# Performance work log

Measured on AMD Instinct MI355X. Metric: run time of the kernel, lower is better.

Reference implementation:

```python
import jax, jax.numpy as jnp
import numpy as np

STRIDE = 32
WINDOW = 16


def setup_inputs() -> dict:
    key = jax.random.key(0)
    kq, kk, kv = jax.random.split(key, 3)
    B, H, S, D = 1, 16, 2048, 64
    q = jax.random.normal(kq, (B, H, S, D), dtype=jnp.float32)
    k = jax.random.normal(kk, (B, H, S, D), dtype=jnp.float32)
    v = jax.random.normal(kv, (B, H, S, D), dtype=jnp.float32)
    return {"q": q, "k": k, "v": v}


def _strided_attention(q, k, v, stride=STRIDE, w=WINDOW):
    b, h, n, d = q.shape
    scale = jnp.asarray(1.0 / np.sqrt(d), dtype=q.dtype)

    # strided (global) tokens: indices 0, stride, 2*stride, ...  [S_str]
    str_idx = jnp.arange(0, n, stride)
    k_str = k[:, :, str_idx, :]  # [b,h,S_str,d]
    v_str = v[:, :, str_idx, :]

    # local window gather: token i attends to j in [i-w, i+w]  (L = 2w+1 slots)
    offs = jnp.arange(-w, w + 1)                      # [L]
    pos = jnp.arange(n)[:, None] + offs[None, :]      # [n, L]
    local_valid = (pos >= 0) & (pos < n)              # [n, L]
    pos_c = jnp.clip(pos, 0, n - 1)
    k_loc = k[:, :, pos_c, :]                         # [b,h,n,L,d]
    v_loc = v[:, :, pos_c, :]                         # [b,h,n,L,d]

    # In the original, strided keys are concatenated ONLY when start > 0,
    # i.e. when i > w (since strided_indices[0] == 0 is inside the window
    # whenever start == 0). Duplicates (strided token inside the local
    # window) are intentionally kept, matching torch.cat semantics.
    use_str = jnp.arange(n) > w                       # [n]

    sc_loc = jnp.einsum('bhnd,bhnld->bhnl', q, k_loc) * scale
    sc_loc = jnp.where(local_valid[None, None], sc_loc, -jnp.inf)
    sc_str = jnp.einsum('bhnd,bhsd->bhns', q, k_str) * scale
    sc_str = jnp.where(use_str[None, None, :, None], sc_str, -jnp.inf)

    L = offs.shape[0]
    attn = jax.nn.softmax(jnp.concatenate([sc_loc, sc_str], axis=-1), axis=-1)
    attn = jnp.nan_to_num(attn, nan=0.0)
    a_loc, a_str = attn[..., :L], attn[..., L:]

    out = jnp.einsum('bhnl,bhnld->bhnd', a_loc, v_loc) \
        + jnp.einsum('bhns,bhsd->bhnd', a_str, v_str)
    return out


def reference(q, k, v):
    return _strided_attention(q, k, v)
```

## Files before the change

### kernel.cpp

```cpp
#include <hip/hip_runtime.h>
#include <math.h>


typedef __attribute__((ext_vector_type(8))) short bf16x8;
typedef __attribute__((ext_vector_type(4))) float f32x4;

constexpr int H = 16, S = 2048, D = 64, W = 16;
constexpr int QB    = 64;
constexpr int NLOC  = 96;
constexpr int NROWS = 160;
constexpr int NT    = 10;
constexpr float SCALE = 0.125f;

constexpr int QSTR = 72;
constexpr int VSTR = 168;
constexpr int QHI  = 0;
constexpr int QLO  = QHI + QB * QSTR;
constexpr int KB   = QLO + QB * QSTR;
constexpr int VTB  = 0;
constexpr int LDS_U = KB + NROWS * QSTR;

__device__ __forceinline__ ushort f2bf(float x) {
    union { float f; unsigned u; } t; t.f = x;
    unsigned r = t.u + 0x7fffu + ((t.u >> 16) & 1u);
    return (ushort)(r >> 16);
}
__device__ __forceinline__ float bf2f(ushort b) {
    union { float f; unsigned u; } t; t.u = ((unsigned)b) << 16;
    return t.f;
}
__device__ __forceinline__ unsigned pk2(float a, float b) {
    return (unsigned)f2bf(a) | ((unsigned)f2bf(b) << 16);
}
__device__ __forceinline__ int rowpos(int r, int n0) {
    if (r < NLOC) {
        int p = n0 - W + r;
        return p < 0 ? 0 : (p > S - 1 ? S - 1 : p);
    }
    return (r - NLOC) * 32;
}

__global__ __launch_bounds__(256, 2) void strided_attn_mfma(
    const float* __restrict__ q,
    const float* __restrict__ k,
    const float* __restrict__ v,
    float* __restrict__ out)
{
    __shared__ ushort lds[LDS_U];

    const int tid  = threadIdx.x;
    const int w    = tid >> 6;
    const int lane = tid & 63;
    const int c    = lane & 15;
    const int g    = lane >> 4;
    const int bid  = blockIdx.x;
    const int swz  = (bid & 7) * 64 + (bid >> 3);
    const int h    = swz >> 5;
    const int n0   = (swz & 31) << 6;

    const float* __restrict__ qh = q + (size_t)(h * S) * D;
    const float* __restrict__ kh = k + (size_t)(h * S) * D;
    const float* __restrict__ vh = v + (size_t)(h * S) * D;

    const int ntask = (tid < 128) ? 3 : 2;
    float4 vreg[3][4];
#pragma unroll
    for (int tt = 0; tt < 3; ++tt) {
        if (tt < ntask) {
            const int tau = tid + (tt << 8);
            const int rp = tau % 80, ch = tau / 80;
            const float* s0 = vh + (size_t)rowpos(2 * rp,     n0) * D + ch * 8;
            const float* s1 = vh + (size_t)rowpos(2 * rp + 1, n0) * D + ch * 8;
            vreg[tt][0] = *(const float4*)s0;
            vreg[tt][1] = *(const float4*)(s0 + 4);
            vreg[tt][2] = *(const float4*)s1;
            vreg[tt][3] = *(const float4*)(s1 + 4);
        }
    }

    for (int t = tid; t < 1792; t += 256) {
        if (t < 512) {
            const int row = t >> 3, ch = t & 7;
            const float* src = qh + (size_t)(n0 + row) * D + ch * 8;
            const float4 a = *(const float4*)src;
            const float4 b = *(const float4*)(src + 4);
            const float xs[8] = {a.x, a.y, a.z, a.w, b.x, b.y, b.z, b.w};
            union { bf16x8 v; ushort u[8]; } hi, lo;
#pragma unroll
            for (int j = 0; j < 8; ++j) {
                const ushort hb = f2bf(xs[j]);
                hi.u[j] = hb;
                lo.u[j] = f2bf(xs[j] - bf2f(hb));
            }
            *(bf16x8*)&lds[QHI + row * QSTR + ch * 8] = hi.v;
            *(bf16x8*)&lds[QLO + row * QSTR + ch * 8] = lo.v;
        } else {
            const int u = t - 512;
            const int row = u >> 3, ch = u & 7;
            const float* src = kh + (size_t)rowpos(row, n0) * D + ch * 8;
            const float4 a = *(const float4*)src;
            const float4 b = *(const float4*)(src + 4);
            const float xs[8] = {a.x, a.y, a.z, a.w, b.x, b.y, b.z, b.w};
            union { bf16x8 v; ushort u[8]; } hi;
#pragma unroll
            for (int j = 0; j < 8; ++j) hi.u[j] = f2bf(xs[j]);
            *(bf16x8*)&lds[KB + row * QSTR + ch * 8] = hi.v;
        }
    }

    unsigned vpk[3][8];
#pragma unroll
    for (int tt = 0; tt < 3; ++tt) {
        if (tt < ntask) {
            const float r0[8] = {vreg[tt][0].x, vreg[tt][0].y, vreg[tt][0].z, vreg[tt][0].w,
                                 vreg[tt][1].x, vreg[tt][1].y, vreg[tt][1].z, vreg[tt][1].w};
            const float r1[8] = {vreg[tt][2].x, vreg[tt][2].y, vreg[tt][2].z, vreg[tt][2].w,
                                 vreg[tt][3].x, vreg[tt][3].y, vreg[tt][3].z, vreg[tt][3].w};
#pragma unroll
            for (int j = 0; j < 8; ++j) vpk[tt][j] = pk2(r0[j], r1[j]);
        }
    }
    __syncthreads();

    const int qb = w * 16;
    const int qi = qb + c;
    const int nq = n0 + qi;
    const int qa = (qb + c) * QSTR + g * 8;
    const bf16x8 bQH0 = *(bf16x8*)&lds[QHI + qa];
    const bf16x8 bQH1 = *(bf16x8*)&lds[QHI + qa + 32];
    const bf16x8 bQL0 = *(bf16x8*)&lds[QLO + qa];
    const bf16x8 bQL1 = *(bf16x8*)&lds[QLO + qa + 32];

    f32x4 acc[NT];
#pragma unroll
    for (int t = 0; t < NT; ++t) acc[t] = (f32x4){0.f, 0.f, 0.f, 0.f};
#pragma unroll
    for (int t = 0; t < NT; ++t) {
        const int kb = KB + (t * 16 + c) * QSTR + g * 8;
        const bf16x8 a0 = *(bf16x8*)&lds[kb];
        const bf16x8 a1 = *(bf16x8*)&lds[kb + 32];
        f32x4 a4 = acc[t];
        a4 = __builtin_amdgcn_mfma_f32_16x16x32_bf16(a0, bQH0, a4, 0, 0, 0);
        a4 = __builtin_amdgcn_mfma_f32_16x16x32_bf16(a1, bQH1, a4, 0, 0, 0);
        a4 = __builtin_amdgcn_mfma_f32_16x16x32_bf16(a0, bQL0, a4, 0, 0, 0);
        a4 = __builtin_amdgcn_mfma_f32_16x16x32_bf16(a1, bQL1, a4, 0, 0, 0);
        acc[t] = a4;
    }

    float p[NT][4];
#pragma unroll
    for (int t = 0; t < 6; ++t) {
#pragma unroll
        for (int i = 0; i < 4; ++i) {
            const int j = t * 16 + 4 * g + i;
            const bool ok = ((unsigned)(j - qi) <= 32u) &&
                            ((unsigned)(n0 - W + j) < (unsigned)S);
            p[t][i] = ok ? acc[t][i] * SCALE : -INFINITY;
        }
    }
    const bool us = nq > W;
#pragma unroll
    for (int t = 6; t < NT; ++t)
#pragma unroll
        for (int i = 0; i < 4; ++i)
            p[t][i] = us ? acc[t][i] * SCALE : -INFINITY;

    float m = -INFINITY;
#pragma unroll
    for (int t = 0; t < NT; ++t)
#pragma unroll
        for (int i = 0; i < 4; ++i) m = fmaxf(m, p[t][i]);
    m = fmaxf(m, __shfl_xor(m, 16));
    m = fmaxf(m, __shfl_xor(m, 32));

    float l = 0.f;
#pragma unroll
    for (int t = 0; t < NT; ++t)
#pragma unroll
        for (int i = 0; i < 4; ++i) { p[t][i] = __expf(p[t][i] - m); l += p[t][i]; }
    l += __shfl_xor(l, 16);
    l += __shfl_xor(l, 32);
    const float inv = 1.0f / l;

    union { bf16x8 v; unsigned u[4]; } pa[5];
#pragma unroll
    for (int kt = 0; kt < 5; ++kt) {
        pa[kt].u[0] = pk2(p[2 * kt][0] * inv,     p[2 * kt][1] * inv);
        pa[kt].u[1] = pk2(p[2 * kt][2] * inv,     p[2 * kt][3] * inv);
        pa[kt].u[2] = pk2(p[2 * kt + 1][0] * inv, p[2 * kt + 1][1] * inv);
        pa[kt].u[3] = pk2(p[2 * kt + 1][2] * inv, p[2 * kt + 1][3] * inv);
    }

    __syncthreads();

#pragma unroll
    for (int tt = 0; tt < 3; ++tt) {
        if (tt < ntask) {
            const int tau = tid + (tt << 8);
            const int rp = tau % 80, ch = tau / 80;
            const int kk = 2 * rp;
            const int kt = kk >> 5, rem = kk & 31;
            const int slot = kt * 32 + ((rem >> 2) & 3) * 8 + (rem >> 4) * 4 + (rem & 3);
#pragma unroll
            for (int j = 0; j < 8; ++j)
                *(unsigned*)&lds[VTB + (ch * 8 + j) * VSTR + slot] = vpk[tt][j];
        }
    }
    __syncthreads();

    f32x4 o[4];
#pragma unroll
    for (int dt = 0; dt < 4; ++dt) o[dt] = (f32x4){0.f, 0.f, 0.f, 0.f};
#pragma unroll
    for (int kt = 0; kt < 5; ++kt) {
#pragma unroll
        for (int dt = 0; dt < 4; ++dt) {
            const bf16x8 vb = *(bf16x8*)&lds[VTB + (dt * 16 + c) * VSTR + kt * 32 + g * 8];
            o[dt] = __builtin_amdgcn_mfma_f32_16x16x32_bf16(pa[kt].v, vb, o[dt], 0, 0, 0);
        }
    }

#pragma unroll
    for (int i = 0; i < 4; ++i) {
        const int n = n0 + qb + 4 * g + i;
        float* op = out + ((size_t)(h * S) + n) * D + c;
#pragma unroll
        for (int dt = 0; dt < 4; ++dt) op[dt * 16] = o[dt][i];
    }
}

extern "C" void kernel_launch(void* const* d_in, const int* in_sizes, int n_in,
                              void* d_out, int out_size, void* d_ws, size_t ws_size,
                              hipStream_t stream) {
    (void)in_sizes; (void)n_in; (void)d_ws; (void)ws_size; (void)out_size;
    const float* q = (const float*)d_in[0];
    const float* k = (const float*)d_in[1];
    const float* v = (const float*)d_in[2];
    float* out     = (float*)d_out;

    dim3 grid(H * (S / QB));
    dim3 block(256);
    strided_attn_mfma<<<grid, block, 0, stream>>>(q, k, v, out);
}
```

Before: 15.33 us.

## Load Q and K fragments directly from global into MFMA registers, skip LDS staging

```diff
diff --git a/kernel.cpp b/kernel.cpp
--- a/kernel.cpp
+++ b/kernel.cpp
@@ -6,19 +6,13 @@
 typedef __attribute__((ext_vector_type(4))) float f32x4;
 
 constexpr int H = 16, S = 2048, D = 64, W = 16;
-constexpr int QB    = 64;
-constexpr int NLOC  = 96;
-constexpr int NROWS = 160;
-constexpr int NT    = 10;
-constexpr float SCALE = 0.125f;
-
-constexpr int QSTR = 72;
-constexpr int VSTR = 168;
-constexpr int QHI  = 0;
-constexpr int QLO  = QHI + QB * QSTR;
-constexpr int KB   = QLO + QB * QSTR;
-constexpr int VTB  = 0;
-constexpr int LDS_U = KB + NROWS * QSTR;
+constexpr int QB   = 64;
+constexpr int NLOC = 96;
+constexpr int NT   = 10;
+constexpr float S2 = 0.18033688011112042f;
+
+constexpr int VSTR  = 168;
+constexpr int LDS_U = D * VSTR;
 
 __device__ __forceinline__ ushort f2bf(float x) {
     union { float f; unsigned u; } t; t.f = x;
@@ -31,6 +25,24 @@
 }
 __device__ __forceinline__ unsigned pk2(float a, float b) {
     return (unsigned)f2bf(a) | ((unsigned)f2bf(b) << 16);
+}
+__device__ __forceinline__ bf16x8 cvt8(const float4& a, const float4& b) {
+    union { bf16x8 v; unsigned u[4]; } r;
+    r.u[0] = pk2(a.x, a.y); r.u[1] = pk2(a.z, a.w);
+    r.u[2] = pk2(b.x, b.y); r.u[3] = pk2(b.z, b.w);
+    return r.v;
+}
+__device__ __forceinline__ void cvt_hilo(const float4& a, const float4& b,
+                                         bf16x8& hi, bf16x8& lo) {
+    const float xs[8] = {a.x, a.y, a.z, a.w, b.x, b.y, b.z, b.w};
+    union { bf16x8 v; ushort u[8]; } Hv, Lv;
+#pragma unroll
+    for (int j = 0; j < 8; ++j) {
+        const ushort hb = f2bf(xs[j]);
+        Hv.u[j] = hb;
+        Lv.u[j] = f2bf(xs[j] - bf2f(hb));
+    }
+    hi = Hv.v; lo = Lv.v;
 }
 __device__ __forceinline__ int rowpos(int r, int n0) {
     if (r < NLOC) {
@@ -78,34 +90,44 @@
         }
     }
 
-    for (int t = tid; t < 1792; t += 256) {
-        if (t < 512) {
-            const int row = t >> 3, ch = t & 7;
-            const float* src = qh + (size_t)(n0 + row) * D + ch * 8;
-            const float4 a = *(const float4*)src;
-            const float4 b = *(const float4*)(src + 4);
-            const float xs[8] = {a.x, a.y, a.z, a.w, b.x, b.y, b.z, b.w};
-            union { bf16x8 v; ushort u[8]; } hi, lo;
-#pragma unroll
-            for (int j = 0; j < 8; ++j) {
-                const ushort hb = f2bf(xs[j]);
-                hi.u[j] = hb;
-                lo.u[j] = f2bf(xs[j] - bf2f(hb));
-            }
-            *(bf16x8*)&lds[QHI + row * QSTR + ch * 8] = hi.v;
-            *(bf16x8*)&lds[QLO + row * QSTR + ch * 8] = lo.v;
+    const int qb = w * 16;
+    const int qi = qb + c;
+    const int nq = n0 + qi;
+    const float* qrow = qh + (size_t)(n0 + qb + c) * D;
+    const float4 qv00 = *(const float4*)(qrow + g * 8);
+    const float4 qv01 = *(const float4*)(qrow + g * 8 + 4);
+    const float4 qv10 = *(const float4*)(qrow + 32 + g * 8);
+    const float4 qv11 = *(const float4*)(qrow + 32 + g * 8 + 4);
+    bf16x8 bQH0, bQL0, bQH1, bQL1;
+    cvt_hilo(qv00, qv01, bQH0, bQL0);
+    cvt_hilo(qv10, qv11, bQH1, bQL1);
+
+    f32x4 acc[NT];
+#pragma unroll
+    for (int t = 0; t < NT; ++t) acc[t] = (f32x4){0.f, 0.f, 0.f, 0.f};
+
+#pragma unroll
+    for (int t = 0; t < NT; ++t) {
+        int pos;
+        if (t < 6) {
+            const int p = n0 - W + 16 * t + c;
+            pos = p < 0 ? 0 : (p > S - 1 ? S - 1 : p);
         } else {
-            const int u = t - 512;
-            const int row = u >> 3, ch = u & 7;
-            const float* src = kh + (size_t)rowpos(row, n0) * D + ch * 8;
-            const float4 a = *(const float4*)src;
-            const float4 b = *(const float4*)(src + 4);
-            const float xs[8] = {a.x, a.y, a.z, a.w, b.x, b.y, b.z, b.w};
-            union { bf16x8 v; ushort u[8]; } hi;
-#pragma unroll
-            for (int j = 0; j < 8; ++j) hi.u[j] = f2bf(xs[j]);
-            *(bf16x8*)&lds[KB + row * QSTR + ch * 8] = hi.v;
-        }
+            pos = (16 * (t - 6) + c) * 32;
+        }
+        const float* kr = kh + (size_t)pos * D;
+        const float4 k00 = *(const float4*)(kr + g * 8);
+        const float4 k01 = *(const float4*)(kr + g * 8 + 4);
+        const float4 k10 = *(const float4*)(kr + 32 + g * 8);
+        const float4 k11 = *(const float4*)(kr + 32 + g * 8 + 4);
+        const bf16x8 a0 = cvt8(k00, k01);
+        const bf16x8 a1 = cvt8(k10, k11);
+        f32x4 a4 = acc[t];
+        a4 = __builtin_amdgcn_mfma_f32_16x16x32_bf16(a0, bQH0, a4, 0, 0, 0);
+        a4 = __builtin_amdgcn_mfma_f32_16x16x32_bf16(a1, bQH1, a4, 0, 0, 0);
+        a4 = __builtin_amdgcn_mfma_f32_16x16x32_bf16(a0, bQL0, a4, 0, 0, 0);
+        a4 = __builtin_amdgcn_mfma_f32_16x16x32_bf16(a1, bQL1, a4, 0, 0, 0);
+        acc[t] = a4;
     }
 
     unsigned vpk[3][8];
@@ -120,79 +142,6 @@
             for (int j = 0; j < 8; ++j) vpk[tt][j] = pk2(r0[j], r1[j]);
         }
     }
-    __syncthreads();
-
-    const int qb = w * 16;
-    const int qi = qb + c;
-    const int nq = n0 + qi;
-    const int qa = (qb + c) * QSTR + g * 8;
-    const bf16x8 bQH0 = *(bf16x8*)&lds[QHI + qa];
-    const bf16x8 bQH1 = *(bf16x8*)&lds[QHI + qa + 32];
-    const bf16x8 bQL0 = *(bf16x8*)&lds[QLO + qa];
-    const bf16x8 bQL1 = *(bf16x8*)&lds[QLO + qa + 32];
-
-    f32x4 acc[NT];
-#pragma unroll
-    for (int t = 0; t < NT; ++t) acc[t] = (f32x4){0.f, 0.f, 0.f, 0.f};
-#pragma unroll
-    for (int t = 0; t < NT; ++t) {
-        const int kb = KB + (t * 16 + c) * QSTR + g * 8;
-        const bf16x8 a0 = *(bf16x8*)&lds[kb];
-        const bf16x8 a1 = *(bf16x8*)&lds[kb + 32];
-        f32x4 a4 = acc[t];
-        a4 = __builtin_amdgcn_mfma_f32_16x16x32_bf16(a0, bQH0, a4, 0, 0, 0);
-        a4 = __builtin_amdgcn_mfma_f32_16x16x32_bf16(a1, bQH1, a4, 0, 0, 0);
-        a4 = __builtin_amdgcn_mfma_f32_16x16x32_bf16(a0, bQL0, a4, 0, 0, 0);
-        a4 = __builtin_amdgcn_mfma_f32_16x16x32_bf16(a1, bQL1, a4, 0, 0, 0);
-        acc[t] = a4;
-    }
-
-    float p[NT][4];
-#pragma unroll
-    for (int t = 0; t < 6; ++t) {
-#pragma unroll
-        for (int i = 0; i < 4; ++i) {
-            const int j = t * 16 + 4 * g + i;
-            const bool ok = ((unsigned)(j - qi) <= 32u) &&
-                            ((unsigned)(n0 - W + j) < (unsigned)S);
-            p[t][i] = ok ? acc[t][i] * SCALE : -INFINITY;
-        }
-    }
-    const bool us = nq > W;
-#pragma unroll
-    for (int t = 6; t < NT; ++t)
-#pragma unroll
-        for (int i = 0; i < 4; ++i)
-            p[t][i] = us ? acc[t][i] * SCALE : -INFINITY;
-
-    float m = -INFINITY;
-#pragma unroll
-    for (int t = 0; t < NT; ++t)
-#pragma unroll
-        for (int i = 0; i < 4; ++i) m = fmaxf(m, p[t][i]);
-    m = fmaxf(m, __shfl_xor(m, 16));
-    m = fmaxf(m, __shfl_xor(m, 32));
-
-    float l = 0.f;
-#pragma unroll
-    for (int t = 0; t < NT; ++t)
-#pragma unroll
-        for (int i = 0; i < 4; ++i) { p[t][i] = __expf(p[t][i] - m); l += p[t][i]; }
-    l += __shfl_xor(l, 16);
-    l += __shfl_xor(l, 32);
-    const float inv = 1.0f / l;
-
-    union { bf16x8 v; unsigned u[4]; } pa[5];
-#pragma unroll
-    for (int kt = 0; kt < 5; ++kt) {
-        pa[kt].u[0] = pk2(p[2 * kt][0] * inv,     p[2 * kt][1] * inv);
-        pa[kt].u[1] = pk2(p[2 * kt][2] * inv,     p[2 * kt][3] * inv);
-        pa[kt].u[2] = pk2(p[2 * kt + 1][0] * inv, p[2 * kt + 1][1] * inv);
-        pa[kt].u[3] = pk2(p[2 * kt + 1][2] * inv, p[2 * kt + 1][3] * inv);
-    }
-
-    __syncthreads();
-
 #pragma unroll
     for (int tt = 0; tt < 3; ++tt) {
         if (tt < ntask) {
@@ -203,9 +152,54 @@
             const int slot = kt * 32 + ((rem >> 2) & 3) * 8 + (rem >> 4) * 4 + (rem & 3);
 #pragma unroll
             for (int j = 0; j < 8; ++j)
-                *(unsigned*)&lds[VTB + (ch * 8 + j) * VSTR + slot] = vpk[tt][j];
-        }
-    }
+                *(unsigned*)&lds[(ch * 8 + j) * VSTR + slot] = vpk[tt][j];
+        }
+    }
+
+    float p[NT][4];
+#pragma unroll
+    for (int t = 0; t < 6; ++t) {
+#pragma unroll
+        for (int i = 0; i < 4; ++i) {
+            const int j = t * 16 + 4 * g + i;
+            const bool ok = ((unsigned)(j - qi) <= 32u) &&
+                            ((unsigned)(n0 - W + j) < (unsigned)S);
+            p[t][i] = ok ? acc[t][i] * S2 : -INFINITY;
+        }
+    }
+    const bool us = nq > W;
+#pragma unroll
+    for (int t = 6; t < NT; ++t)
+#pragma unroll
+        for (int i = 0; i < 4; ++i)
+            p[t][i] = us ? acc[t][i] * S2 : -INFINITY;
+
+    float m = -INFINITY;
+#pragma unroll
+    for (int t = 0; t < NT; ++t)
+#pragma unroll
+        for (int i = 0; i < 4; ++i) m = fmaxf(m, p[t][i]);
+    m = fmaxf(m, __shfl_xor(m, 16));
+    m = fmaxf(m, __shfl_xor(m, 32));
+
+    float l = 0.f;
+#pragma unroll
+    for (int t = 0; t < NT; ++t)
+#pragma unroll
+        for (int i = 0; i < 4; ++i) { p[t][i] = exp2f(p[t][i] - m); l += p[t][i]; }
+    l += __shfl_xor(l, 16);
+    l += __shfl_xor(l, 32);
+    const float inv = 1.0f / l;
+
+    union { bf16x8 v; unsigned u[4]; } pa[5];
+#pragma unroll
+    for (int kt = 0; kt < 5; ++kt) {
+        pa[kt].u[0] = pk2(p[2 * kt][0] * inv,     p[2 * kt][1] * inv);
+        pa[kt].u[1] = pk2(p[2 * kt][2] * inv,     p[2 * kt][3] * inv);
+        pa[kt].u[2] = pk2(p[2 * kt + 1][0] * inv, p[2 * kt + 1][1] * inv);
+        pa[kt].u[3] = pk2(p[2 * kt + 1][2] * inv, p[2 * kt + 1][3] * inv);
+    }
+
     __syncthreads();
 
     f32x4 o[4];
@@ -215,7 +209,7 @@
     for (int kt = 0; kt < 5; ++kt) {
 #pragma unroll
         for (int dt = 0; dt < 4; ++dt) {
-            const bf16x8 vb = *(bf16x8*)&lds[VTB + (dt * 16 + c) * VSTR + kt * 32 + g * 8];
+            const bf16x8 vb = *(bf16x8*)&lds[(dt * 16 + c) * VSTR + kt * 32 + g * 8];
             o[dt] = __builtin_amdgcn_mfma_f32_16x16x32_bf16(pa[kt].v, vb, o[dt], 0, 0, 0);
         }
     }
```

Measured after the change: 23.28 us. +51.9%, slower.

## Halve query tile to 32 rows, fold scale into Q, use exp2

Applied to the files above, without the earlier changes.

```diff
diff --git a/kernel.cpp b/kernel.cpp
--- a/kernel.cpp
+++ b/kernel.cpp
@@ -6,14 +6,14 @@
 typedef __attribute__((ext_vector_type(4))) float f32x4;
 
 constexpr int H = 16, S = 2048, D = 64, W = 16;
-constexpr int QB    = 64;
-constexpr int NLOC  = 96;
-constexpr int NROWS = 160;
-constexpr int NT    = 10;
-constexpr float SCALE = 0.125f;
+constexpr int QB    = 32;
+constexpr int NLOC  = 64;
+constexpr int NROWS = 128;
+constexpr int NT    = 8;
+constexpr float S2 = 0.18033688011112042f;
 
 constexpr int QSTR = 72;
-constexpr int VSTR = 168;
+constexpr int VSTR = 136;
 constexpr int QHI  = 0;
 constexpr int QLO  = QHI + QB * QSTR;
 constexpr int KB   = QLO + QB * QSTR;
@@ -32,6 +32,12 @@
 __device__ __forceinline__ unsigned pk2(float a, float b) {
     return (unsigned)f2bf(a) | ((unsigned)f2bf(b) << 16);
 }
+__device__ __forceinline__ bf16x8 cvt8(const float4& a, const float4& b) {
+    union { bf16x8 v; unsigned u[4]; } r;
+    r.u[0] = pk2(a.x, a.y); r.u[1] = pk2(a.z, a.w);
+    r.u[2] = pk2(b.x, b.y); r.u[3] = pk2(b.z, b.w);
+    return r.v;
+}
 __device__ __forceinline__ int rowpos(int r, int n0) {
     if (r < NLOC) {
         int p = n0 - W + r;
@@ -40,7 +46,7 @@
     return (r - NLOC) * 32;
 }
 
-__global__ __launch_bounds__(256, 2) void strided_attn_mfma(
+__global__ __launch_bounds__(128, 2) void strided_attn_mfma(
     const float* __restrict__ q,
     const float* __restrict__ k,
     const float* __restrict__ v,
@@ -54,37 +60,35 @@
     const int c    = lane & 15;
     const int g    = lane >> 4;
     const int bid  = blockIdx.x;
-    const int swz  = (bid & 7) * 64 + (bid >> 3);
-    const int h    = swz >> 5;
-    const int n0   = (swz & 31) << 6;
+    const int swz  = (bid & 7) * 128 + (bid >> 3);
+    const int h    = swz >> 6;
+    const int n0   = (swz & 63) << 5;
 
     const float* __restrict__ qh = q + (size_t)(h * S) * D;
     const float* __restrict__ kh = k + (size_t)(h * S) * D;
     const float* __restrict__ vh = v + (size_t)(h * S) * D;
 
-    const int ntask = (tid < 128) ? 3 : 2;
-    float4 vreg[3][4];
-#pragma unroll
-    for (int tt = 0; tt < 3; ++tt) {
-        if (tt < ntask) {
-            const int tau = tid + (tt << 8);
-            const int rp = tau % 80, ch = tau / 80;
-            const float* s0 = vh + (size_t)rowpos(2 * rp,     n0) * D + ch * 8;
-            const float* s1 = vh + (size_t)rowpos(2 * rp + 1, n0) * D + ch * 8;
-            vreg[tt][0] = *(const float4*)s0;
-            vreg[tt][1] = *(const float4*)(s0 + 4);
-            vreg[tt][2] = *(const float4*)s1;
-            vreg[tt][3] = *(const float4*)(s1 + 4);
-        }
-    }
-
-    for (int t = tid; t < 1792; t += 256) {
-        if (t < 512) {
+    float4 vreg[4][4];
+#pragma unroll
+    for (int tt = 0; tt < 4; ++tt) {
+        const int tau = tid + (tt << 7);
+        const int rp = tau & 63, ch = tau >> 6;
+        const float* s0 = vh + (size_t)rowpos(2 * rp,     n0) * D + ch * 8;
+        const float* s1 = vh + (size_t)rowpos(2 * rp + 1, n0) * D + ch * 8;
+        vreg[tt][0] = *(const float4*)s0;
+        vreg[tt][1] = *(const float4*)(s0 + 4);
+        vreg[tt][2] = *(const float4*)s1;
+        vreg[tt][3] = *(const float4*)(s1 + 4);
+    }
+
+    for (int t = tid; t < 1280; t += 128) {
+        if (t < 256) {
             const int row = t >> 3, ch = t & 7;
             const float* src = qh + (size_t)(n0 + row) * D + ch * 8;
             const float4 a = *(const float4*)src;
             const float4 b = *(const float4*)(src + 4);
-            const float xs[8] = {a.x, a.y, a.z, a.w, b.x, b.y, b.z, b.w};
+            const float xs[8] = {a.x * S2, a.y * S2, a.z * S2, a.w * S2,
+                                 b.x * S2, b.y * S2, b.z * S2, b.w * S2};
             union { bf16x8 v; ushort u[8]; } hi, lo;
 #pragma unroll
             for (int j = 0; j < 8; ++j) {
@@ -95,29 +99,12 @@
             *(bf16x8*)&lds[QHI + row * QSTR + ch * 8] = hi.v;
             *(bf16x8*)&lds[QLO + row * QSTR + ch * 8] = lo.v;
         } else {
-            const int u = t - 512;
+            const int u = t - 256;
             const int row = u >> 3, ch = u & 7;
             const float* src = kh + (size_t)rowpos(row, n0) * D + ch * 8;
             const float4 a = *(const float4*)src;
             const float4 b = *(const float4*)(src + 4);
-            const float xs[8] = {a.x, a.y, a.z, a.w, b.x, b.y, b.z, b.w};
-            union { bf16x8 v; ushort u[8]; } hi;
-#pragma unroll
-            for (int j = 0; j < 8; ++j) hi.u[j] = f2bf(xs[j]);
-            *(bf16x8*)&lds[KB + row * QSTR + ch * 8] = hi.v;
-        }
-    }
-
-    unsigned vpk[3][8];
-#pragma unroll
-    for (int tt = 0; tt < 3; ++tt) {
-        if (tt < ntask) {
-            const float r0[8] = {vreg[tt][0].x, vreg[tt][0].y, vreg[tt][0].z, vreg[tt][0].w,
-                                 vreg[tt][1].x, vreg[tt][1].y, vreg[tt][1].z, vreg[tt][1].w};
-            const float r1[8] = {vreg[tt][2].x, vreg[tt][2].y, vreg[tt][2].z, vreg[tt][2].w,
-                                 vreg[tt][3].x, vreg[tt][3].y, vreg[tt][3].z, vreg[tt][3].w};
-#pragma unroll
-            for (int j = 0; j < 8; ++j) vpk[tt][j] = pk2(r0[j], r1[j]);
+            *(bf16x8*)&lds[KB + row * QSTR + ch * 8] = cvt8(a, b);
         }
     }
     __syncthreads();
@@ -149,21 +136,21 @@
 
     float p[NT][4];
 #pragma unroll
-    for (int t = 0; t < 6; ++t) {
+    for (int t = 0; t < 4; ++t) {
 #pragma unroll
         for (int i = 0; i < 4; ++i) {
             const int j = t * 16 + 4 * g + i;
             const bool ok = ((unsigned)(j - qi) <= 32u) &&
                             ((unsigned)(n0 - W + j) < (unsigned)S);
-            p[t][i] = ok ? acc[t][i] * SCALE : -INFINITY;
+            p[t][i] = ok ? acc[t][i] : -INFINITY;
         }
     }
     const bool us = nq > W;
 #pragma unroll
-    for (int t = 6; t < NT; ++t)
+    for (int t = 4; t < NT; ++t)
 #pragma unroll
         for (int i = 0; i < 4; ++i)
-            p[t][i] = us ? acc[t][i] * SCALE : -INFINITY;
+            p[t][i] = us ? acc[t][i] : -INFINITY;
 
     float m = -INFINITY;
 #pragma unroll
@@ -177,14 +164,14 @@
 #pragma unroll
     for (int t = 0; t < NT; ++t)
 #pragma unroll
-        for (int i = 0; i < 4; ++i) { p[t][i] = __expf(p[t][i] - m); l += p[t][i]; }
+        for (int i = 0; i < 4; ++i) { p[t][i] = exp2f(p[t][i] - m); l += p[t][i]; }
     l += __shfl_xor(l, 16);
     l += __shfl_xor(l, 32);
     const float inv = 1.0f / l;
 
-    union { bf16x8 v; unsigned u[4]; } pa[5];
-#pragma unroll
-    for (int kt = 0; kt < 5; ++kt) {
+    union { bf16x8 v; unsigned u[4]; } pa[4];
+#pragma unroll
+    for (int kt = 0; kt < 4; ++kt) {
         pa[kt].u[0] = pk2(p[2 * kt][0] * inv,     p[2 * kt][1] * inv);
         pa[kt].u[1] = pk2(p[2 * kt][2] * inv,     p[2 * kt][3] * inv);
         pa[kt].u[2] = pk2(p[2 * kt + 1][0] * inv, p[2 * kt + 1][1] * inv);
@@ -194,17 +181,19 @@
     __syncthreads();
 
 #pragma unroll
-    for (int tt = 0; tt < 3; ++tt) {
-        if (tt < ntask) {
-            const int tau = tid + (tt << 8);
-            const int rp = tau % 80, ch = tau / 80;
-            const int kk = 2 * rp;
-            const int kt = kk >> 5, rem = kk & 31;
-            const int slot = kt * 32 + ((rem >> 2) & 3) * 8 + (rem >> 4) * 4 + (rem & 3);
-#pragma unroll
-            for (int j = 0; j < 8; ++j)
-                *(unsigned*)&lds[VTB + (ch * 8 + j) * VSTR + slot] = vpk[tt][j];
-        }
+    for (int tt = 0; tt < 4; ++tt) {
+        const int tau = tid + (tt << 7);
+        const int rp = tau & 63, ch = tau >> 6;
+        const float r0[8] = {vreg[tt][0].x, vreg[tt][0].y, vreg[tt][0].z, vreg[tt][0].w,
+                             vreg[tt][1].x, vreg[tt][1].y, vreg[tt][1].z, vreg[tt][1].w};
+        const float r1[8] = {vreg[tt][2].x, vreg[tt][2].y, vreg[tt][2].z, vreg[tt][2].w,
+                             vreg[tt][3].x, vreg[tt][3].y, vreg[tt][3].z, vreg[tt][3].w};
+        const int kk = 2 * rp;
+        const int kt = kk >> 5, rem = kk & 31;
+        const int slot = kt * 32 + ((rem >> 2) & 3) * 8 + (rem >> 4) * 4 + (rem & 3);
+#pragma unroll
+        for (int j = 0; j < 8; ++j)
+            *(unsigned*)&lds[VTB + (ch * 8 + j) * VSTR + slot] = pk2(r0[j], r1[j]);
     }
     __syncthreads();
 
@@ -212,7 +201,7 @@
 #pragma unroll
     for (int dt = 0; dt < 4; ++dt) o[dt] = (f32x4){0.f, 0.f, 0.f, 0.f};
 #pragma unroll
-    for (int kt = 0; kt < 5; ++kt) {
+    for (int kt = 0; kt < 4; ++kt) {
 #pragma unroll
         for (int dt = 0; dt < 4; ++dt) {
             const bf16x8 vb = *(bf16x8*)&lds[VTB + (dt * 16 + c) * VSTR + kt * 32 + g * 8];
@@ -239,6 +228,6 @@
     float* out     = (float*)d_out;
 
     dim3 grid(H * (S / QB));
-    dim3 block(256);
+    dim3 block(128);
     strided_attn_mfma<<<grid, block, 0, stream>>>(q, k, v, out);
 }
```

Result: slower. 17.76 us (+15.9%).
